# Optimization experiments

Hardware: AMD Instinct MI355X
Metric: run time of the kernel (lower is better)

The kernel has to match this reference:

```python
import jax, jax.numpy as jnp
import numpy as np

N = 50000          # nodes
E = 1_600_000      # edges (avg degree 32)
IN_DIM = 1024
HID = 32           # int(sqrt(IN_DIM))
OUT_DIMS = (2, 3)  # multi-task classifier heads


def setup_inputs() -> dict:
    key = jax.random.key(0)
    ks = jax.random.split(key, 16)
    x = jax.random.normal(ks[0], (N, IN_DIM), dtype=jnp.float32)
    adj_rows = jax.random.randint(ks[1], (E,), 0, N, dtype=jnp.int32)
    adj_cols = jax.random.randint(ks[2], (E,), 0, N, dtype=jnp.int32)
    adj_vals = jax.random.uniform(ks[3], (E,), dtype=jnp.float32) / 32.0  # ~normalized adj

    def xn(k, fan_in, fan_out, gain=0.75):  # xavier_normal with gain 3/4 (selu_xn)
        std = gain * np.sqrt(2.0 / (fan_in + fan_out))
        return jax.random.normal(k, (fan_in, fan_out), dtype=jnp.float32) * std

    w1 = xn(ks[4], IN_DIM, HID)
    w2 = xn(ks[5], HID, HID)
    w3 = xn(ks[6], HID, HID)
    b1 = jnp.zeros((HID,), jnp.float32)
    b2 = jnp.zeros((HID,), jnp.float32)
    b3 = jnp.zeros((HID,), jnp.float32)
    # clf heads: nn.Linear(HID, num_class), xavier_normal gain 1, zero bias
    clf_w0 = xn(ks[7], HID, OUT_DIMS[0], gain=1.0).T  # stored torch-style [out, in]
    clf_w1 = xn(ks[8], HID, OUT_DIMS[1], gain=1.0).T
    clf_b0 = jnp.zeros((OUT_DIMS[0],), jnp.float32)
    clf_b1 = jnp.zeros((OUT_DIMS[1],), jnp.float32)
    return {"x": x, "adj_rows": adj_rows, "adj_cols": adj_cols, "adj_vals": adj_vals,
            "w1": w1, "b1": b1, "w2": w2, "b2": b2, "w3": w3, "b3": b3,
            "clf_w0": clf_w0, "clf_b0": clf_b0, "clf_w1": clf_w1, "clf_b1": clf_b1}


def reference(x, adj_rows, adj_cols, adj_vals, w1, b1, w2, b2, w3, b3,
              clf_w0, clf_b0, clf_w1, clf_b1):
    def gcn_layer(h, w, b):
        support = h @ w                                   # [N, out]
        msgs = adj_vals[:, None] * support[adj_cols]      # gather along edges
        agg = jax.ops.segment_sum(msgs, adj_rows, num_segments=N)  # SpMM
        # eval mode: UniformDropout is identity; then SELU, then bias add
        return jax.nn.selu(agg) + b

    h = gcn_layer(x, w1, b1)
    h = gcn_layer(h, w2, b2)
    h = gcn_layer(h, w3, b3)
    out0 = h @ clf_w0.T + clf_b0   # [N, 2]
    out1 = h @ clf_w1.T + clf_b1   # [N, 3]
    return (out0, out1)
```

## Files before the change

### kernel.cpp

```cpp
#include <hip/hip_runtime.h>

#define IN_DIM 1024
#define HID 32
#define BSHIFT 5
#define BROWS 32
#define MAXB 1600
#define NBLK 64
#define SORT_CAP 4096

__device__ __forceinline__ float selu_f(float x) {
    const float scale = 1.0507009873554805f;
    const float alpha = 1.6732632423543772f;
    return x > 0.f ? scale * x : scale * alpha * (expf(x) - 1.f);
}


__global__ __launch_bounds__(1024) void part_hist(const int* __restrict__ rows, int E, int NB,
                                                  int nchunk, int* __restrict__ counts) {
    __shared__ int lh[MAXB];
    int tid = threadIdx.x, blk = blockIdx.x;
    for (int b = tid; b < NB; b += 1024) lh[b] = 0;
    __syncthreads();
    int base = blk * nchunk;
    int end = base + nchunk; if (end > E) end = E;
    for (int i = base + tid; i < end; i += 1024)
        atomicAdd(&lh[rows[i] >> BSHIFT], 1);
    __syncthreads();
    for (int b = tid; b < NB; b += 1024) counts[b * NBLK + blk] = lh[b];
}

__global__ __launch_bounds__(1024) void scan1_kernel(const int* __restrict__ in, int n,
                                                     int* __restrict__ out,
                                                     int* __restrict__ partials) {
    __shared__ int s[1024];
    int tid = threadIdx.x;
    int i = blockIdx.x * 1024 + tid;
    int v = (i < n) ? in[i] : 0;
    s[tid] = v;
    __syncthreads();
    for (int off = 1; off < 1024; off <<= 1) {
        int t = (tid >= off) ? s[tid - off] : 0;
        __syncthreads();
        s[tid] += t;
        __syncthreads();
    }
    if (i < n) out[i] = s[tid] - v;
    if (tid == 1023) partials[blockIdx.x] = s[tid];
}

__global__ void scan2_kernel(int* __restrict__ partials, int nb) {
    __shared__ int s[128];
    int tid = threadIdx.x;
    int v = (tid < nb) ? partials[tid] : 0;
    s[tid] = v;
    __syncthreads();
    for (int off = 1; off < 128; off <<= 1) {
        int t = (tid >= off) ? s[tid - off] : 0;
        __syncthreads();
        s[tid] += t;
        __syncthreads();
    }
    if (tid < nb) partials[tid] = s[tid] - v;
}

__global__ __launch_bounds__(1024) void scan3_kernel(int* __restrict__ out,
                                                     const int* __restrict__ partials, int n) {
    int i = blockIdx.x * 1024 + threadIdx.x;
    if (i < n) out[i] += partials[blockIdx.x];
}

__global__ __launch_bounds__(1024) void part_scatter(const int* __restrict__ rows,
                                                     const int* __restrict__ cols,
                                                     const float* __restrict__ vals, int E,
                                                     int NB, int nchunk,
                                                     const int* __restrict__ offs,
                                                     int2* __restrict__ edata) {
    __shared__ int lc[MAXB];
    int tid = threadIdx.x, blk = blockIdx.x;
    for (int b = tid; b < NB; b += 1024) lc[b] = offs[b * NBLK + blk];
    __syncthreads();
    int base = blk * nchunk;
    int end = base + nchunk; if (end > E) end = E;
    for (int i = base + tid; i < end; i += 1024) {
        int r = rows[i];
        int b = r >> BSHIFT;
        int p = atomicAdd(&lc[b], 1);
        int2 pr;
        pr.x = ((r & (BROWS - 1)) << 18) | cols[i];
        pr.y = __float_as_int(vals[i]);
        edata[p] = pr;
    }
}

__global__ __launch_bounds__(256) void bucket_sort(int2* __restrict__ edata,
                                                   const int* __restrict__ offs,
                                                   int E, int NB,
                                                   int* __restrict__ rowptr) {
    __shared__ int2 stage[SORT_CAP];
    __shared__ int cnt[32], startsh[32], cur[32];
    int b = blockIdx.x, tid = threadIdx.x;
    int s0 = offs[b * NBLK];
    int s1 = (b + 1 < NB) ? offs[(b + 1) * NBLK] : E;
    int n = s1 - s0;
    if (tid < 32) cnt[tid] = 0;
    __syncthreads();
    for (int i = tid; i < n; i += 256) {
        int2 pr = edata[s0 + i];
        stage[i] = pr;
        atomicAdd(&cnt[pr.x >> 18], 1);
    }
    __syncthreads();
    if (tid == 0) {
        int run = 0;
        #pragma unroll
        for (int k = 0; k < 32; ++k) { startsh[k] = run; run += cnt[k]; }
    }
    __syncthreads();
    if (tid < 32) {
        cur[tid] = startsh[tid];
        rowptr[b * BROWS + tid] = s0 + startsh[tid];
    }
    __syncthreads();
    for (int i = tid; i < n; i += 256) {
        int2 pr = stage[i];
        int p = atomicAdd(&cur[pr.x >> 18], 1);
        edata[s0 + p] = pr;
    }
}


#define XS_LD 132

__global__ __launch_bounds__(256) void gemm1_kernel(const float* __restrict__ x,
                                                    const float* __restrict__ w,
                                                    float* __restrict__ out, int N) {
    __shared__ float xs[32 * XS_LD];
    __shared__ float ws[128 * HID];
    int tid = threadIdx.x;
    int r  = tid >> 3;
    int d0 = (tid & 7) * 4;
    int row0 = blockIdx.x * 32;

    float4 acc = make_float4(0.f, 0.f, 0.f, 0.f);

    for (int kc = 0; kc < IN_DIM; kc += 128) {
        #pragma unroll
        for (int j = 0; j < 4; ++j) {
            int linear = tid + j * 256;
            int rr = linear >> 5;
            int cc = linear & 31;
            int grow = row0 + rr;
            if (grow > N - 1) grow = N - 1;
            float4 t = *(const float4*)&x[(size_t)grow * IN_DIM + kc + cc * 4];
            *(float4*)&xs[rr * XS_LD + cc * 4] = t;
        }
        #pragma unroll
        for (int j = 0; j < 4; ++j) {
            int linear = tid + j * 256;
            int kk = linear >> 3;
            int dd = (linear & 7) * 4;
            float4 t = *(const float4*)&w[(kc + kk) * HID + dd];
            *(float4*)&ws[kk * HID + dd] = t;
        }
        __syncthreads();
        #pragma unroll
        for (int k4 = 0; k4 < 32; ++k4) {
            float4 xv = *(const float4*)&xs[r * XS_LD + k4 * 4];
            float4 wv0 = *(const float4*)&ws[(k4 * 4 + 0) * HID + d0];
            acc.x += xv.x * wv0.x; acc.y += xv.x * wv0.y; acc.z += xv.x * wv0.z; acc.w += xv.x * wv0.w;
            float4 wv1 = *(const float4*)&ws[(k4 * 4 + 1) * HID + d0];
            acc.x += xv.y * wv1.x; acc.y += xv.y * wv1.y; acc.z += xv.y * wv1.z; acc.w += xv.y * wv1.w;
            float4 wv2 = *(const float4*)&ws[(k4 * 4 + 2) * HID + d0];
            acc.x += xv.z * wv2.x; acc.y += xv.z * wv2.y; acc.z += xv.z * wv2.z; acc.w += xv.z * wv2.w;
            float4 wv3 = *(const float4*)&ws[(k4 * 4 + 3) * HID + d0];
            acc.x += xv.w * wv3.x; acc.y += xv.w * wv3.y; acc.z += xv.w * wv3.z; acc.w += xv.w * wv3.w;
        }
        __syncthreads();
    }
    int grow = row0 + r;
    if (grow < N) *(float4*)&out[(size_t)grow * HID + d0] = acc;
}


__device__ __forceinline__ float4 spmm_row_f4(const float4* __restrict__ sup4,
                                              const int2* __restrict__ edata,
                                              int e0, int e1, int l) {
    float4 a0 = {0.f,0.f,0.f,0.f}, a1 = a0, a2 = a0, a3 = a0;
    int e = e0;
    for (; e + 4 <= e1; e += 4) {
        int2 m0 = edata[e], m1 = edata[e+1], m2 = edata[e+2], m3 = edata[e+3];
        float4 g0 = sup4[(size_t)(m0.x & 0x3FFFF) * 8 + l];
        float4 g1 = sup4[(size_t)(m1.x & 0x3FFFF) * 8 + l];
        float4 g2 = sup4[(size_t)(m2.x & 0x3FFFF) * 8 + l];
        float4 g3 = sup4[(size_t)(m3.x & 0x3FFFF) * 8 + l];
        float v0 = __int_as_float(m0.y), v1 = __int_as_float(m1.y);
        float v2 = __int_as_float(m2.y), v3 = __int_as_float(m3.y);
        a0.x += v0*g0.x; a0.y += v0*g0.y; a0.z += v0*g0.z; a0.w += v0*g0.w;
        a1.x += v1*g1.x; a1.y += v1*g1.y; a1.z += v1*g1.z; a1.w += v1*g1.w;
        a2.x += v2*g2.x; a2.y += v2*g2.y; a2.z += v2*g2.z; a2.w += v2*g2.w;
        a3.x += v3*g3.x; a3.y += v3*g3.y; a3.z += v3*g3.z; a3.w += v3*g3.w;
    }
    for (; e < e1; ++e) {
        int2 m0 = edata[e];
        float4 g0 = sup4[(size_t)(m0.x & 0x3FFFF) * 8 + l];
        float v0 = __int_as_float(m0.y);
        a0.x += v0*g0.x; a0.y += v0*g0.y; a0.z += v0*g0.z; a0.w += v0*g0.w;
    }
    a0.x += a1.x + a2.x + a3.x;
    a0.y += a1.y + a2.y + a3.y;
    a0.z += a1.z + a2.z + a3.z;
    a0.w += a1.w + a2.w + a3.w;
    return a0;
}

__global__ __launch_bounds__(256) void spmm_mid_kernel(const float4* __restrict__ sup4,
                                                       const int* __restrict__ rowptr,
                                                       const int2* __restrict__ edata,
                                                       int N,
                                                       const float* __restrict__ bias,
                                                       const float* __restrict__ Wn,
                                                       float* __restrict__ out) {
    __shared__ float Wsh[HID * HID];
    __shared__ float hs[BROWS][36];
    int tid = threadIdx.x;
    int b = blockIdx.x;
    *(float4*)&Wsh[tid * 4] = ((const float4*)Wn)[tid];
    int g = tid >> 3, l = tid & 7;
    int row = b * BROWS + g;
    float4 acc = {0.f,0.f,0.f,0.f};
    if (row < N) {
        int e0 = rowptr[row];
        int e1 = rowptr[row + 1];
        acc = spmm_row_f4(sup4, edata, e0, e1, l);
    }
    float4 b4 = ((const float4*)bias)[l];
    float4 h;
    h.x = selu_f(acc.x) + b4.x;
    h.y = selu_f(acc.y) + b4.y;
    h.z = selu_f(acc.z) + b4.z;
    h.w = selu_f(acc.w) + b4.w;
    *(float4*)&hs[g][l * 4] = h;
    __syncthreads();
    int d = tid & 31;
    #pragma unroll
    for (int k = 0; k < 4; ++k) {
        int rl = (tid >> 5) + k * 8;
        int rrow = b * BROWS + rl;
        float o = 0.f;
        #pragma unroll
        for (int j = 0; j < HID; ++j) o += hs[rl][j] * Wsh[j * HID + d];
        if (rrow < N) out[(size_t)rrow * HID + d] = o;
    }
}

__global__ __launch_bounds__(256) void spmm_final_kernel(const float4* __restrict__ sup4,
                                                         const int* __restrict__ rowptr,
                                                         const int2* __restrict__ edata,
                                                         int N,
                                                         const float* __restrict__ bias,
                                                         const float* __restrict__ cw0,
                                                         const float* __restrict__ cb0,
                                                         const float* __restrict__ cw1,
                                                         const float* __restrict__ cb1,
                                                         float* __restrict__ out) {
    __shared__ float hs[BROWS][36];
    int tid = threadIdx.x;
    int b = blockIdx.x;
    int g = tid >> 3, l = tid & 7;
    int row = b * BROWS + g;
    float4 acc = {0.f,0.f,0.f,0.f};
    if (row < N) {
        int e0 = rowptr[row];
        int e1 = rowptr[row + 1];
        acc = spmm_row_f4(sup4, edata, e0, e1, l);
    }
    float4 b4 = ((const float4*)bias)[l];
    float4 h;
    h.x = selu_f(acc.x) + b4.x;
    h.y = selu_f(acc.y) + b4.y;
    h.z = selu_f(acc.z) + b4.z;
    h.w = selu_f(acc.w) + b4.w;
    *(float4*)&hs[g][l * 4] = h;
    __syncthreads();
    if (tid < BROWS * 5) {
        int rl = tid / 5, t = tid % 5;
        int rrow = b * BROWS + rl;
        if (rrow < N) {
            if (t < 2) {
                float o = cb0[t];
                #pragma unroll
                for (int j = 0; j < HID; ++j) o += hs[rl][j] * cw0[t * HID + j];
                out[(size_t)rrow * 2 + t] = o;
            } else {
                int c = t - 2;
                float o = cb1[c];
                #pragma unroll
                for (int j = 0; j < HID; ++j) o += hs[rl][j] * cw1[c * HID + j];
                out[(size_t)N * 2 + (size_t)rrow * 3 + c] = o;
            }
        }
    }
}


extern "C" void kernel_launch(void* const* d_in, const int* in_sizes, int n_in,
                              void* d_out, int out_size, void* d_ws, size_t ws_size,
                              hipStream_t stream) {
    const float* x        = (const float*)d_in[0];
    const int*   adj_rows = (const int*)d_in[1];
    const int*   adj_cols = (const int*)d_in[2];
    const float* adj_vals = (const float*)d_in[3];
    const float* w1 = (const float*)d_in[4];
    const float* b1 = (const float*)d_in[5];
    const float* w2 = (const float*)d_in[6];
    const float* b2 = (const float*)d_in[7];
    const float* w3 = (const float*)d_in[8];
    const float* b3 = (const float*)d_in[9];
    const float* cw0 = (const float*)d_in[10];
    const float* cb0 = (const float*)d_in[11];
    const float* cw1 = (const float*)d_in[12];
    const float* cb1 = (const float*)d_in[13];

    int N = in_sizes[0] / IN_DIM;
    int E = in_sizes[1];
    int NB = (N + BROWS - 1) >> BSHIFT;
    int M = NB * NBLK;
    int nchunk = (E + NBLK - 1) / NBLK;
    int nb1 = (M + 1023) / 1024;

    char* p = (char*)d_ws;
    float* s_a   = (float*)p; p += (size_t)N * HID * sizeof(float);
    float* s_b   = (float*)p; p += (size_t)N * HID * sizeof(float);
    int2*  edata = (int2*)p;  p += (size_t)E * sizeof(int2);
    int*   counts   = (int*)p; p += (size_t)M * sizeof(int);
    int*   offs     = (int*)p; p += (size_t)M * sizeof(int);
    int*   rowptr   = (int*)p; p += (size_t)(NB * BROWS + 1) * sizeof(int);
    int*   partials = (int*)p; p += 128 * sizeof(int);

    part_hist<<<NBLK, 1024, 0, stream>>>(adj_rows, E, NB, nchunk, counts);
    scan1_kernel<<<nb1, 1024, 0, stream>>>(counts, M, offs, partials);
    scan2_kernel<<<1, 128, 0, stream>>>(partials, nb1);
    scan3_kernel<<<nb1, 1024, 0, stream>>>(offs, partials, M);
    part_scatter<<<NBLK, 1024, 0, stream>>>(adj_rows, adj_cols, adj_vals, E, NB, nchunk,
                                            offs, edata);
    bucket_sort<<<NB, 256, 0, stream>>>(edata, offs, E, NB, rowptr);

    gemm1_kernel<<<(N + 31) / 32, 256, 0, stream>>>(x, w1, s_a, N);
    spmm_mid_kernel<<<NB, 256, 0, stream>>>((const float4*)s_a, rowptr, edata, N, b1, w2, s_b);
    spmm_mid_kernel<<<NB, 256, 0, stream>>>((const float4*)s_b, rowptr, edata, N, b2, w3, s_a);
    spmm_final_kernel<<<NB, 256, 0, stream>>>((const float4*)s_a, rowptr, edata, N,
                                              b3, cw0, cb0, cw1, cb1, (float*)d_out);
}
```

Baseline: 496.1 us.

## Double partition blocks, fuse scan passes, deepen SpMM gather unroll

Measured after the change: 475.4 us. 4.2% less time.

```diff
diff --git a/kernel.cpp b/kernel.cpp
--- a/kernel.cpp
+++ b/kernel.cpp
@@ -5,7 +5,7 @@
 #define BSHIFT 5
 #define BROWS 32
 #define MAXB 1600
-#define NBLK 64
+#define NBLK 128
 #define SORT_CAP 4096
 
 __device__ __forceinline__ float selu_f(float x) {
@@ -26,16 +26,22 @@
     for (int i = base + tid; i < end; i += 1024)
         atomicAdd(&lh[rows[i] >> BSHIFT], 1);
     __syncthreads();
-    for (int b = tid; b < NB; b += 1024) counts[b * NBLK + blk] = lh[b];
-}
-
-__global__ __launch_bounds__(1024) void scan1_kernel(const int* __restrict__ in, int n,
-                                                     int* __restrict__ out,
+    for (int b = tid; b < NB; b += 1024) counts[blk * NB + b] = lh[b];
+}
+
+__global__ __launch_bounds__(1024) void scan1_kernel(const int* __restrict__ counts, int M,
+                                                     int NB,
+                                                     int* __restrict__ offs,
                                                      int* __restrict__ partials) {
     __shared__ int s[1024];
     int tid = threadIdx.x;
     int i = blockIdx.x * 1024 + tid;
-    int v = (i < n) ? in[i] : 0;
+    int v = 0;
+    if (i < M) {
+        int b = i >> 7;
+        int blk = i & (NBLK - 1);
+        v = counts[blk * NB + b];
+    }
     s[tid] = v;
     __syncthreads();
     for (int off = 1; off < 1024; off <<= 1) {
@@ -44,29 +50,27 @@
         s[tid] += t;
         __syncthreads();
     }
-    if (i < n) out[i] = s[tid] - v;
+    if (i < M) offs[i] = s[tid] - v;
     if (tid == 1023) partials[blockIdx.x] = s[tid];
 }
 
-__global__ void scan2_kernel(int* __restrict__ partials, int nb) {
-    __shared__ int s[128];
-    int tid = threadIdx.x;
-    int v = (tid < nb) ? partials[tid] : 0;
-    s[tid] = v;
-    __syncthreads();
-    for (int off = 1; off < 128; off <<= 1) {
-        int t = (tid >= off) ? s[tid - off] : 0;
-        __syncthreads();
-        s[tid] += t;
-        __syncthreads();
-    }
-    if (tid < nb) partials[tid] = s[tid] - v;
-}
-
-__global__ __launch_bounds__(1024) void scan3_kernel(int* __restrict__ out,
-                                                     const int* __restrict__ partials, int n) {
-    int i = blockIdx.x * 1024 + threadIdx.x;
-    if (i < n) out[i] += partials[blockIdx.x];
+__global__ __launch_bounds__(1024) void scan_fix_kernel(int* __restrict__ offs,
+                                                        const int* __restrict__ partials,
+                                                        int M, int nb1) {
+    __shared__ int s[256];
+    int tid = threadIdx.x;
+    if (tid < 256) s[tid] = (tid < nb1) ? partials[tid] : 0;
+    __syncthreads();
+    for (int off = 1; off < 256; off <<= 1) {
+        int t = 0;
+        if (tid < 256 && tid >= off) t = s[tid - off];
+        __syncthreads();
+        if (tid < 256) s[tid] += t;
+        __syncthreads();
+    }
+    int myoff = (blockIdx.x == 0) ? 0 : s[blockIdx.x - 1];
+    int i = blockIdx.x * 1024 + tid;
+    if (i < M) offs[i] += myoff;
 }
 
 __global__ __launch_bounds__(1024) void part_scatter(const int* __restrict__ rows,
@@ -187,18 +191,29 @@
                                               int e0, int e1, int l) {
     float4 a0 = {0.f,0.f,0.f,0.f}, a1 = a0, a2 = a0, a3 = a0;
     int e = e0;
-    for (; e + 4 <= e1; e += 4) {
-        int2 m0 = edata[e], m1 = edata[e+1], m2 = edata[e+2], m3 = edata[e+3];
+    for (; e + 8 <= e1; e += 8) {
+        int2 m0 = edata[e],   m1 = edata[e+1], m2 = edata[e+2], m3 = edata[e+3];
+        int2 m4 = edata[e+4], m5 = edata[e+5], m6 = edata[e+6], m7 = edata[e+7];
         float4 g0 = sup4[(size_t)(m0.x & 0x3FFFF) * 8 + l];
         float4 g1 = sup4[(size_t)(m1.x & 0x3FFFF) * 8 + l];
         float4 g2 = sup4[(size_t)(m2.x & 0x3FFFF) * 8 + l];
         float4 g3 = sup4[(size_t)(m3.x & 0x3FFFF) * 8 + l];
+        float4 g4 = sup4[(size_t)(m4.x & 0x3FFFF) * 8 + l];
+        float4 g5 = sup4[(size_t)(m5.x & 0x3FFFF) * 8 + l];
+        float4 g6 = sup4[(size_t)(m6.x & 0x3FFFF) * 8 + l];
+        float4 g7 = sup4[(size_t)(m7.x & 0x3FFFF) * 8 + l];
         float v0 = __int_as_float(m0.y), v1 = __int_as_float(m1.y);
         float v2 = __int_as_float(m2.y), v3 = __int_as_float(m3.y);
+        float v4 = __int_as_float(m4.y), v5 = __int_as_float(m5.y);
+        float v6 = __int_as_float(m6.y), v7 = __int_as_float(m7.y);
         a0.x += v0*g0.x; a0.y += v0*g0.y; a0.z += v0*g0.z; a0.w += v0*g0.w;
         a1.x += v1*g1.x; a1.y += v1*g1.y; a1.z += v1*g1.z; a1.w += v1*g1.w;
         a2.x += v2*g2.x; a2.y += v2*g2.y; a2.z += v2*g2.z; a2.w += v2*g2.w;
         a3.x += v3*g3.x; a3.y += v3*g3.y; a3.z += v3*g3.z; a3.w += v3*g3.w;
+        a0.x += v4*g4.x; a0.y += v4*g4.y; a0.z += v4*g4.z; a0.w += v4*g4.w;
+        a1.x += v5*g5.x; a1.y += v5*g5.y; a1.z += v5*g5.z; a1.w += v5*g5.w;
+        a2.x += v6*g6.x; a2.y += v6*g6.y; a2.z += v6*g6.z; a2.w += v6*g6.w;
+        a3.x += v7*g7.x; a3.y += v7*g7.y; a3.z += v7*g7.z; a3.w += v7*g7.w;
     }
     for (; e < e1; ++e) {
         int2 m0 = edata[e];
@@ -335,12 +350,11 @@
     int*   counts   = (int*)p; p += (size_t)M * sizeof(int);
     int*   offs     = (int*)p; p += (size_t)M * sizeof(int);
     int*   rowptr   = (int*)p; p += (size_t)(NB * BROWS + 1) * sizeof(int);
-    int*   partials = (int*)p; p += 128 * sizeof(int);
+    int*   partials = (int*)p; p += 256 * sizeof(int);
 
     part_hist<<<NBLK, 1024, 0, stream>>>(adj_rows, E, NB, nchunk, counts);
-    scan1_kernel<<<nb1, 1024, 0, stream>>>(counts, M, offs, partials);
-    scan2_kernel<<<1, 128, 0, stream>>>(partials, nb1);
-    scan3_kernel<<<nb1, 1024, 0, stream>>>(offs, partials, M);
+    scan1_kernel<<<nb1, 1024, 0, stream>>>(counts, M, NB, offs, partials);
+    scan_fix_kernel<<<nb1, 1024, 0, stream>>>(offs, partials, M, nb1);
     part_scatter<<<NBLK, 1024, 0, stream>>>(adj_rows, adj_cols, adj_vals, E, NB, nchunk,
                                             offs, edata);
     bucket_sort<<<NB, 256, 0, stream>>>(edata, offs, E, NB, rowptr);
```
